# Optimization experiments

Measured on AMD Instinct MI355X. Metric: run time of the kernel, lower is better.

## Reference

```python
import jax, jax.numpy as jnp
import numpy as np

B, S, SE, D, H = 4, 1024, 256, 1536, 24
HD = D // H
EPS = 1e-5
STYLE_IDX = np.array([0, 0, 2, 2])  # expand_first: style stats of sample 0 -> {0,1}, sample 2 -> {2,3}


def adain(feat):
    # feat: [B,H,S,hd]; stats over seq dim (-2), unbiased var like torch
    m = feat.mean(axis=-2, keepdims=True)
    s = jnp.sqrt(feat.var(axis=-2, keepdims=True, ddof=1) + EPS)
    sm, ss = m[STYLE_IDX], s[STYLE_IDX]
    styled = (feat - m) / s * ss + sm
    # only batch indices 1 and 3 are restyled
    mask = jnp.array([0.0, 1.0, 0.0, 1.0], dtype=feat.dtype).reshape(B, 1, 1, 1)
    return feat * (1.0 - mask) + styled * mask


def heads(x):
    b, s, _ = x.shape
    return x.reshape(b, s, H, HD).transpose(0, 2, 1, 3)


def setup_inputs() -> dict:
    key = jax.random.key(0)
    ks = jax.random.split(key, 12)
    w = lambda k: jax.random.normal(k, (D, D), dtype=jnp.float32) * 0.02
    z = jnp.zeros((D,), dtype=jnp.float32)
    return {
        'hidden_states': jax.random.normal(ks[0], (B, S, D), dtype=jnp.float32),
        'encoder_hidden_states': jax.random.normal(ks[1], (B, SE, D), dtype=jnp.float32),
        'wq': w(ks[2]), 'bq': z, 'wk': w(ks[3]), 'bk': z, 'wv': w(ks[4]), 'bv': z,
        'awq': w(ks[5]), 'abq': z, 'awk': w(ks[6]), 'abk': z, 'awv': w(ks[7]), 'abv': z,
        'wo': w(ks[8]), 'bo': z, 'wao': w(ks[9]), 'bao': z,
    }


def reference(hidden_states, encoder_hidden_states, wq, bq, wk, bk, wv, bv,
              awq, abq, awk, abk, awv, abv, wo, bo, wao, bao):
    q = heads(hidden_states @ wq + bq)   # [B,H,S,hd]
    k = heads(hidden_states @ wk + bk)
    v = heads(hidden_states @ wv + bv)
    # adain_queries / adain_keys (adain_values=False)
    q = adain(q)
    k = adain(k)
    # share_attention: concat style K/V (scale=1.0 -> plain expand) along seq
    k = jnp.concatenate([k, k[STYLE_IDX]], axis=2)  # [B,H,2S,hd]
    v = jnp.concatenate([v, v[STYLE_IDX]], axis=2)
    # joint (text) streams
    eq = heads(encoder_hidden_states @ awq + abq)
    ek = heads(encoder_hidden_states @ awk + abk)
    ev = heads(encoder_hidden_states @ awv + abv)
    q = jnp.concatenate([q, eq], axis=2)   # [B,H,S+SE,hd]
    k = jnp.concatenate([k, ek], axis=2)   # [B,H,2S+SE,hd]
    v = jnp.concatenate([v, ev], axis=2)
    scale = 1.0 / np.sqrt(HD)
    logits = jnp.einsum('bhqd,bhkd->bhqk', q, k) * scale
    probs = jax.nn.softmax(logits, axis=-1)
    out = jnp.einsum('bhqk,bhkd->bhqd', probs, v)
    out = out.transpose(0, 2, 1, 3).reshape(B, -1, D)
    hid, enc = out[:, :S], out[:, S:]
    hid = hid @ wo + bo            # to_out[0] (to_out[1] is dropout/identity)
    enc = enc @ wao + bao          # to_add_out (context_pre_only=False)
    return hid, enc
```

## Files before the change

kernel.cpp:

```cpp
#include <hip/hip_runtime.h>
#include <hip/hip_bf16.h>


#define NB 4
#define NS 1024
#define NSE 256
#define ND 1536
#define NH 24
#define LK2 1280
#define SMAX 20.0f

typedef short bf16x8 __attribute__((ext_vector_type(8)));
typedef float f32x4 __attribute__((ext_vector_type(4)));

struct WPtrs { const float* w[8]; };
struct B6    { const float* p[6]; };

__device__ __forceinline__ unsigned short f2bf(float x) {
  union { float f; unsigned u; } a; a.f = x;
  unsigned r = a.u + 0x7fffu + ((a.u >> 16) & 1u);
  return (unsigned short)(r >> 16);
}
__device__ __forceinline__ void split2(float x, unsigned short& h, unsigned short& l) {
  union { float f; unsigned u; } a; a.f = x;
  h = (unsigned short)(a.u >> 16);
  union { float f; unsigned u; } b; b.u = a.u & 0xffff0000u;
  union { float f; unsigned u; } c; c.f = x - b.f;
  l = (unsigned short)(c.u >> 16);
}

__device__ __forceinline__ void gload_lds16(const unsigned short* g, unsigned short* l) {
  __builtin_amdgcn_global_load_lds(
      (const __attribute__((address_space(1))) void*)g,
      (__attribute__((address_space(3))) void*)l, 16, 0, 0);
}

__global__ __launch_bounds__(256) void conv_split_all(
    const float* __restrict__ hs, const float* __restrict__ ehs,
    unsigned short* __restrict__ HSh, unsigned short* __restrict__ HSl,
    unsigned short* __restrict__ EHh, unsigned short* __restrict__ EHl)
{
  int i = blockIdx.x * 256 + threadIdx.x;
  const float4* src; ushort4 *dh, *dl; int j;
  if (i < 1572864) { src = (const float4*)hs; j = i; dh = (ushort4*)HSh; dl = (ushort4*)HSl; }
  else { j = i - 1572864; src = (const float4*)ehs; dh = (ushort4*)EHh; dl = (ushort4*)EHl; }
  float4 v = src[j];
  ushort4 h, lo;
  split2(v.x, h.x, lo.x); split2(v.y, h.y, lo.y);
  split2(v.z, h.z, lo.z); split2(v.w, h.w, lo.w);
  dh[j] = h; dl[j] = lo;
}

__global__ __launch_bounds__(256) void conv_wt_all(WPtrs wp,
                                                   unsigned short* __restrict__ Wsp)
{
  __shared__ float tile[32][33];
  const int z = blockIdx.z;
  const float* W = wp.w[z];
  unsigned short* Th = Wsp + (long)(2 * z) * 2359296;
  unsigned short* Tl = Th + 2359296;
  const int k0 = blockIdx.x * 32, n0 = blockIdx.y * 32;
  const int r = threadIdx.x >> 5, c = threadIdx.x & 31;
#pragma unroll
  for (int i = 0; i < 4; ++i)
    tile[r + 8 * i][c] = W[(long)(k0 + r + 8 * i) * ND + n0 + c];
  __syncthreads();
#pragma unroll
  for (int i = 0; i < 4; ++i) {
    float v = tile[c][r + 8 * i];
    long o = (long)(n0 + r + 8 * i) * ND + k0 + c;
    unsigned short h, l;
    split2(v, h, l);
    Th[o] = h; Tl[o] = l;
  }
}

__device__ __forceinline__ void gemm_mfma_body(
    const unsigned short* __restrict__ Ah, const unsigned short* __restrict__ Al,
    const unsigned short* __restrict__ Bh, const unsigned short* __restrict__ Bl,
    const float* __restrict__ bias, float* __restrict__ C, int m0, int n0,
    bool third)
{
  __shared__ unsigned short sAh[128 * 32], sAl[128 * 32];
  __shared__ unsigned short sBh[128 * 32], sBl[128 * 32];

  const int t = threadIdx.x;
  const int w = t >> 6, l = t & 63;

  const int lr = l >> 2;
  const int lc = (l & 3) * 8;

  const unsigned short* pAh = Ah + (long)(m0 + 32 * w + lr) * ND + lc;
  const unsigned short* pAl = Al + (long)(m0 + 32 * w + lr) * ND + lc;
  const unsigned short* pBh = Bh + (long)(n0 + 32 * w + lr) * ND + lc;
  const unsigned short* pBl = Bl + (long)(n0 + 32 * w + lr) * ND + lc;

  unsigned short* qAh0 = &sAh[(32 * w) * 32];
  unsigned short* qAh1 = &sAh[(32 * w + 16) * 32];
  unsigned short* qAl0 = &sAl[(32 * w) * 32];
  unsigned short* qAl1 = &sAl[(32 * w + 16) * 32];
  unsigned short* qBh0 = &sBh[(32 * w) * 32];
  unsigned short* qBh1 = &sBh[(32 * w + 16) * 32];
  unsigned short* qBl0 = &sBl[(32 * w) * 32];
  unsigned short* qBl1 = &sBl[(32 * w + 16) * 32];

  const int rowA = (w >> 1) * 64 + (l & 15);
  const int rowB = (w & 1) * 64 + (l & 15);
  const int ko = (l >> 4) * 8;

  f32x4 acc[4][4] = {};

  for (int k0 = 0; k0 < ND; k0 += 32) {
    gload_lds16(pAh, qAh0);
    gload_lds16(pAh + 16 * ND, qAh1);
    if (third) {
      gload_lds16(pAl, qAl0);
      gload_lds16(pAl + 16 * ND, qAl1);
    }
    gload_lds16(pBh, qBh0);
    gload_lds16(pBh + 16 * ND, qBh1);
    gload_lds16(pBl, qBl0);
    gload_lds16(pBl + 16 * ND, qBl1);
    pAh += 32; pAl += 32; pBh += 32; pBl += 32;
    __syncthreads();

    bf16x8 fah[4], fal[4], fbh[4], fbl[4];
#pragma unroll
    for (int mt = 0; mt < 4; ++mt)
      fah[mt] = *(const bf16x8*)&sAh[(rowA + mt * 16) * 32 + ko];
    if (third) {
#pragma unroll
      for (int mt = 0; mt < 4; ++mt)
        fal[mt] = *(const bf16x8*)&sAl[(rowA + mt * 16) * 32 + ko];
    }
#pragma unroll
    for (int nt = 0; nt < 4; ++nt) {
      fbh[nt] = *(const bf16x8*)&sBh[(rowB + nt * 16) * 32 + ko];
      fbl[nt] = *(const bf16x8*)&sBl[(rowB + nt * 16) * 32 + ko];
    }
#pragma unroll
    for (int mt = 0; mt < 4; ++mt)
#pragma unroll
      for (int nt = 0; nt < 4; ++nt) {
        acc[mt][nt] = __builtin_amdgcn_mfma_f32_16x16x32_bf16(fah[mt], fbh[nt], acc[mt][nt], 0, 0, 0);
        acc[mt][nt] = __builtin_amdgcn_mfma_f32_16x16x32_bf16(fah[mt], fbl[nt], acc[mt][nt], 0, 0, 0);
      }
    if (third) {
#pragma unroll
      for (int mt = 0; mt < 4; ++mt)
#pragma unroll
        for (int nt = 0; nt < 4; ++nt)
          acc[mt][nt] = __builtin_amdgcn_mfma_f32_16x16x32_bf16(fal[mt], fbh[nt], acc[mt][nt], 0, 0, 0);
    }
    __syncthreads();
  }

  const int col0 = n0 + (w & 1) * 64 + (l & 15);
  const int row0 = m0 + (w >> 1) * 64 + (l >> 4) * 4;
#pragma unroll
  for (int nt = 0; nt < 4; ++nt) {
    float bv = bias[col0 + nt * 16];
#pragma unroll
    for (int mt = 0; mt < 4; ++mt)
#pragma unroll
      for (int r = 0; r < 4; ++r)
        C[(long)(row0 + mt * 16 + r) * ND + col0 + nt * 16] = acc[mt][nt][r] + bv;
  }
}

__global__ __launch_bounds__(256) void gemm3_all(
    const unsigned short* __restrict__ HSh, const unsigned short* __restrict__ HSl,
    const unsigned short* __restrict__ EHh, const unsigned short* __restrict__ EHl,
    const unsigned short* __restrict__ Wsp, B6 biases,
    float* __restrict__ Qb, float* __restrict__ EQb)
{
  const int z = blockIdx.z, y = blockIdx.y;
  const unsigned short *Ah, *Al;
  float* C;
  int m0, widx;
  if (y < 32) { Ah = HSh; Al = HSl; m0 = y * 128; widx = z;
                C = Qb + (long)z * 6291456; }
  else        { Ah = EHh; Al = EHl; m0 = (y - 32) * 128; widx = 3 + z;
                C = EQb + (long)z * 1572864; }
  const unsigned short* Bh = Wsp + (long)(2 * widx) * 2359296;
  const unsigned short* Bl = Bh + 2359296;
  gemm_mfma_body(Ah, Al, Bh, Bl, biases.p[widx], C, m0, blockIdx.x * 128,
                 z == 2);
}

__global__ __launch_bounds__(256) void gemm_out_all(
    const unsigned short* __restrict__ AOh,
    const unsigned short* __restrict__ Wsp,
    const float* __restrict__ bo, const float* __restrict__ bao,
    float* __restrict__ out)
{
  const int z = blockIdx.z, y = blockIdx.y;
  const unsigned short *Ah, *Bh, *Bl;
  const float* bias;
  float* C;
  int m0;
  if (y < 8) {
    Ah = AOh + (long)z * 1966080;
    m0 = y * 128;
    Bh = Wsp + (long)12 * 2359296; Bl = Bh + 2359296;
    bias = bo; C = out + (long)z * 1572864;
  } else {
    Ah = AOh + 1572864 + (long)z * 1966080;
    m0 = (y - 8) * 128;
    Bh = Wsp + (long)14 * 2359296; Bl = Bh + 2359296;
    bias = bao; C = out + 6291456 + (long)z * 393216;
  }
  gemm_mfma_body(Ah, Ah, Bh, Bl, bias, C, m0, blockIdx.x * 128, false);
}

__global__ __launch_bounds__(256) void adain_stats2(
    const float* __restrict__ Qb, const float* __restrict__ Kb,
    float* __restrict__ stm, float* __restrict__ sts,
    float* __restrict__ stm2, float* __restrict__ sts2)
{
  const float* X = blockIdx.z ? Kb : Qb;
  float* meanb = blockIdx.z ? stm2 : stm;
  float* sigb  = blockIdx.z ? sts2 : sts;
  const int b  = blockIdx.x;
  const int t  = threadIdx.x;
  const int dl = t & 63;
  const int sg = t >> 6;
  const int d  = blockIdx.y * 64 + dl;
  const float* xp = X + (long)b * NS * ND + d;
  float sum = 0.f, sq = 0.f;
  for (int s = sg; s < NS; s += 4) {
    float v = xp[(long)s * ND];
    sum += v; sq += v * v;
  }
  __shared__ float ss[4][64], s2[4][64];
  ss[sg][dl] = sum; s2[sg][dl] = sq;
  __syncthreads();
  if (t < 64) {
    float tot = ss[0][t] + ss[1][t] + ss[2][t] + ss[3][t];
    float tq  = s2[0][t] + s2[1][t] + s2[2][t] + s2[3][t];
    float mean = tot * (1.f / 1024.f);
    float var  = (tq - tot * mean) * (1.f / 1023.f);
    meanb[b * ND + blockIdx.y * 64 + t] = mean;
    sigb [b * ND + blockIdx.y * 64 + t] = sqrtf(var + 1e-5f);
  }
}

__global__ __launch_bounds__(256) void conv_KV(
    const float* __restrict__ Kf, const float* __restrict__ EKf,
    const float* __restrict__ Vf, const float* __restrict__ EVf,
    const float* __restrict__ stm2, const float* __restrict__ sts2,
    unsigned short* __restrict__ Kh, unsigned short* __restrict__ Kl,
    unsigned short* __restrict__ VT)
{
  __shared__ float tile[64][65];
  const int bh = blockIdx.y, b = bh / NH, h = bh - b * NH;
  if (blockIdx.x < 20) {
    const int key = blockIdx.x * 64 + (threadIdx.x >> 2);
    const int dc = (threadIdx.x & 3) * 16;
    const bool kad = ((b & 1) != 0) && (key < NS);
    const int srcb = b & 2;
    const float* src = (key < NS)
        ? Kf  + ((long)b * NS + key) * ND + h * 64 + dc
        : EKf + ((long)b * NSE + key - NS) * ND + h * 64 + dc;
    unsigned short* dh = Kh + ((long)bh * LK2 + key) * 64 + dc;
    unsigned short* dl = Kl + ((long)bh * LK2 + key) * 64 + dc;
    const long sb = (long)b * ND + h * 64 + dc;
    const long ss = (long)srcb * ND + h * 64 + dc;
#pragma unroll
    for (int i = 0; i < 4; ++i) {
      float4 v = *(const float4*)(src + 4 * i);
      if (kad) {
        float4 mb = *(const float4*)(stm2 + sb + 4 * i);
        float4 gb = *(const float4*)(sts2 + sb + 4 * i);
        float4 ms = *(const float4*)(stm2 + ss + 4 * i);
        float4 gs = *(const float4*)(sts2 + ss + 4 * i);
        v.x = (v.x - mb.x) * (gs.x / gb.x) + ms.x;
        v.y = (v.y - mb.y) * (gs.y / gb.y) + ms.y;
        v.z = (v.z - mb.z) * (gs.z / gb.z) + ms.z;
        v.w = (v.w - mb.w) * (gs.w / gb.w) + ms.w;
      }
      ushort4 hi, lo;
      split2(v.x, hi.x, lo.x); split2(v.y, hi.y, lo.y);
      split2(v.z, hi.z, lo.z); split2(v.w, hi.w, lo.w);
      *(ushort4*)(dh + 4 * i) = hi;
      *(ushort4*)(dl + 4 * i) = lo;
    }
  } else {
    const int k0 = (blockIdx.x - 20) * 64;
    {
      const int kl_ = threadIdx.x >> 2, dc = (threadIdx.x & 3) * 16;
      const int key = k0 + kl_;
      const float* src = (key < NS)
          ? Vf  + ((long)b * NS + key) * ND + h * 64 + dc
          : EVf + ((long)b * NSE + key - NS) * ND + h * 64 + dc;
#pragma unroll
      for (int i = 0; i < 4; ++i) {
        float4 v = *(const float4*)(src + 4 * i);
        tile[kl_][dc + 4 * i + 0] = v.x; tile[kl_][dc + 4 * i + 1] = v.y;
        tile[kl_][dc + 4 * i + 2] = v.z; tile[kl_][dc + 4 * i + 3] = v.w;
      }
    }
    __syncthreads();
    const int d = threadIdx.x >> 2, kc = (threadIdx.x & 3) * 16;
    unsigned short* dst = VT + ((long)bh * 64 + d) * LK2 + k0 + kc;
#pragma unroll
    for (int i = 0; i < 4; ++i) {
      ushort4 o4;
      o4.x = f2bf(tile[kc + 4 * i + 0][d]);
      o4.y = f2bf(tile[kc + 4 * i + 1][d]);
      o4.z = f2bf(tile[kc + 4 * i + 2][d]);
      o4.w = f2bf(tile[kc + 4 * i + 3][d]);
      *(ushort4*)(dst + 4 * i) = o4;
    }
  }
}

__global__ __launch_bounds__(256) void attn_mfma(
    const float* __restrict__ Q, const float* __restrict__ EQ,
    const unsigned short* __restrict__ Khg, const unsigned short* __restrict__ Klg,
    const unsigned short* __restrict__ VTg,
    const float* __restrict__ stm, const float* __restrict__ sts,
    unsigned short* __restrict__ AOh)
{
  __shared__ unsigned short sKh[2][64 * 64], sKl[2][64 * 64], sVT[2][64 * 64];
  __shared__ unsigned short sPh[64 * 72], sPl[64 * 72];

  const int t = threadIdx.x, w = t >> 6, l = t & 63;
  const int bh = blockIdx.y, b = bh / NH, h = bh - b * NH;
  const int bhs = (b & 2) * NH + h;
  const int q0 = blockIdx.x * 64;
  const int m = l & 15, g = l >> 4;
  const bool beven = (b & 1) == 0;
  const int nIter = beven ? 20 : 36;

  union FU { bf16x8 v; unsigned short u[8]; };
  FU qh[2], ql[2];
  {
    const bool qad = !beven && (q0 < NS);
    const int srcb = b & 2;
    const float* qrow = (q0 < NS)
        ? (Q  + ((long)b * NS + q0 + 16 * w + m) * ND + h * 64)
        : (EQ + ((long)b * NSE + (q0 - NS) + 16 * w + m) * ND + h * 64);
#pragma unroll
    for (int ks = 0; ks < 2; ++ks) {
      const int d0 = h * 64 + ks * 32 + g * 8;
      const float* p = qrow + ks * 32 + g * 8;
      float4 v0 = *(const float4*)p, v1 = *(const float4*)(p + 4);
      float vv[8] = {v0.x, v0.y, v0.z, v0.w, v1.x, v1.y, v1.z, v1.w};
      if (qad) {
        float4 mb0 = *(const float4*)(stm + (long)b * ND + d0);
        float4 mb1 = *(const float4*)(stm + (long)b * ND + d0 + 4);
        float4 gb0 = *(const float4*)(sts + (long)b * ND + d0);
        float4 gb1 = *(const float4*)(sts + (long)b * ND + d0 + 4);
        float4 ms0 = *(const float4*)(stm + (long)srcb * ND + d0);
        float4 ms1 = *(const float4*)(stm + (long)srcb * ND + d0 + 4);
        float4 gs0 = *(const float4*)(sts + (long)srcb * ND + d0);
        float4 gs1 = *(const float4*)(sts + (long)srcb * ND + d0 + 4);
        float mb[8] = {mb0.x, mb0.y, mb0.z, mb0.w, mb1.x, mb1.y, mb1.z, mb1.w};
        float gb[8] = {gb0.x, gb0.y, gb0.z, gb0.w, gb1.x, gb1.y, gb1.z, gb1.w};
        float ms[8] = {ms0.x, ms0.y, ms0.z, ms0.w, ms1.x, ms1.y, ms1.z, ms1.w};
        float gs[8] = {gs0.x, gs0.y, gs0.z, gs0.w, gs1.x, gs1.y, gs1.z, gs1.w};
#pragma unroll
        for (int j = 0; j < 8; ++j)
          vv[j] = (vv[j] - mb[j]) * (gs[j] / gb[j]) + ms[j];
      }
#pragma unroll
      for (int j = 0; j < 8; ++j)
        split2(vv[j] * 0.125f, qh[ks].u[j], ql[ks].u[j]);
    }
  }

  const int srow = l >> 3;
  const int sp = l & 7;
  const int osw = (sp - srow) & 7;
  const long ownK = (long)bh * LK2 * 64, styK = (long)bhs * LK2 * 64;
  const long ownV = (long)bh * 64 * LK2, styV = (long)bhs * 64 * LK2;
  const int offK = (16 * w + srow) * 64 + osw * 8;
  const int offV = (16 * w + srow) * LK2 + osw * 8;

  auto stage = [&](int kt, int bi) {
    int zone, j;
    if (beven) { zone = (kt < 16) ? 0 : 2; j = (kt < 16) ? kt : kt - 16; }
    else {
      zone = (kt < 16) ? 0 : ((kt < 32) ? 1 : 2);
      j = (kt < 16) ? kt : ((kt < 32) ? kt - 16 : kt - 32);
    }
    const long keyBase = ((zone == 2) ? 1024 : 0) + (long)j * 64;
    const unsigned short* kb = Khg + ((zone == 1) ? styK : ownK) + keyBase * 64;
    const unsigned short* lb = Klg + ((zone == 1) ? styK : ownK) + keyBase * 64;
    const unsigned short* vb = VTg + ((zone == 1) ? styV : ownV) + keyBase;
    gload_lds16(kb + offK, &sKh[bi][(16 * w) * 64]);
    gload_lds16(kb + 8 * 64 + offK, &sKh[bi][(16 * w + 8) * 64]);
    gload_lds16(lb + offK, &sKl[bi][(16 * w) * 64]);
    gload_lds16(lb + 8 * 64 + offK, &sKl[bi][(16 * w + 8) * 64]);
    gload_lds16(vb + offV, &sVT[bi][(16 * w) * 64]);
    gload_lds16(vb + 8 * LK2 + offV, &sVT[bi][(16 * w + 8) * 64]);
  };

  const int p0 = (g + m) & 7;
  const int p1 = (4 + g + m) & 7;

  f32x4 oacc[4] = {};
  float l_part[4] = {0.f, 0.f, 0.f, 0.f};

  stage(0, 0);

  for (int kt = 0; kt < nIter; ++kt) {
    const int cur = kt & 1;
    __syncthreads();
    if (kt + 1 < nIter) stage(kt + 1, cur ^ 1);

    const float ebias = (beven && kt < 16) ? (0.69314718f - SMAX) : (-SMAX);

    f32x4 sacc[4] = {};
#pragma unroll
    for (int ks = 0; ks < 2; ++ks) {
      const int pp = ks ? p1 : p0;
#pragma unroll
      for (int nt = 0; nt < 4; ++nt) {
        const int ak = (nt * 16 + m) * 64 + pp * 8;
        bf16x8 fkh = *(const bf16x8*)&sKh[cur][ak];
        bf16x8 fkl = *(const bf16x8*)&sKl[cur][ak];
        sacc[nt] = __builtin_amdgcn_mfma_f32_16x16x32_bf16(qh[ks].v, fkh, sacc[nt], 0, 0, 0);
        sacc[nt] = __builtin_amdgcn_mfma_f32_16x16x32_bf16(qh[ks].v, fkl, sacc[nt], 0, 0, 0);
        sacc[nt] = __builtin_amdgcn_mfma_f32_16x16x32_bf16(ql[ks].v, fkh, sacc[nt], 0, 0, 0);
      }
    }

#pragma unroll
    for (int nt = 0; nt < 4; ++nt)
#pragma unroll
      for (int r = 0; r < 4; ++r)
        sacc[nt][r] = __expf(sacc[nt][r] + ebias);
#pragma unroll
    for (int r = 0; r < 4; ++r)
      l_part[r] += (sacc[0][r] + sacc[1][r]) + (sacc[2][r] + sacc[3][r]);
#pragma unroll
    for (int nt = 0; nt < 4; ++nt)
#pragma unroll
      for (int r = 0; r < 4; ++r) {
        unsigned short ph, pl;
        split2(sacc[nt][r], ph, pl);
        const int ad = (16 * w + 4 * g + r) * 72 + nt * 16 + m;
        sPh[ad] = ph; sPl[ad] = pl;
      }

#pragma unroll
    for (int ks = 0; ks < 2; ++ks) {
      const int pp = ks ? p1 : p0;
      const int ap = (16 * w + m) * 72 + ks * 32 + g * 8;
      bf16x8 fph = *(const bf16x8*)&sPh[ap];
      bf16x8 fpl = *(const bf16x8*)&sPl[ap];
#pragma unroll
      for (int nt2 = 0; nt2 < 4; ++nt2) {
        const int av = (nt2 * 16 + m) * 64 + pp * 8;
        bf16x8 fv = *(const bf16x8*)&sVT[cur][av];
        oacc[nt2] = __builtin_amdgcn_mfma_f32_16x16x32_bf16(fph, fv, oacc[nt2], 0, 0, 0);
        oacc[nt2] = __builtin_amdgcn_mfma_f32_16x16x32_bf16(fpl, fv, oacc[nt2], 0, 0, 0);
      }
    }
  }

#pragma unroll
  for (int r = 0; r < 4; ++r) {
#pragma unroll
    for (int off = 1; off < 16; off <<= 1)
      l_part[r] += __shfl_xor(l_part[r], off, 16);
  }
#pragma unroll
  for (int r = 0; r < 4; ++r) {
    float inv = 1.f / l_part[r];
    const long row = (long)b * 1280 + q0 + 16 * w + 4 * g + r;
    const long base = row * ND + h * 64;
#pragma unroll
    for (int nt2 = 0; nt2 < 4; ++nt2)
      AOh[base + nt2 * 16 + m] = f2bf(oacc[nt2][r] * inv);
  }
}

extern "C" void kernel_launch(void* const* d_in, const int* in_sizes, int n_in,
                              void* d_out, int out_size, void* d_ws, size_t ws_size,
                              hipStream_t stream) {
  const float* hs  = (const float*)d_in[0];
  const float* ehs = (const float*)d_in[1];
  WPtrs wp;
  wp.w[0] = (const float*)d_in[2];  wp.w[1] = (const float*)d_in[4];
  wp.w[2] = (const float*)d_in[6];  wp.w[3] = (const float*)d_in[8];
  wp.w[4] = (const float*)d_in[10]; wp.w[5] = (const float*)d_in[12];
  wp.w[6] = (const float*)d_in[14]; wp.w[7] = (const float*)d_in[16];
  B6 biases;
  biases.p[0] = (const float*)d_in[3];
  biases.p[1] = (const float*)d_in[5];
  biases.p[2] = (const float*)d_in[7];
  biases.p[3] = (const float*)d_in[9];
  biases.p[4] = (const float*)d_in[11];
  biases.p[5] = (const float*)d_in[13];
  const float* bo  = (const float*)d_in[15];
  const float* bao = (const float*)d_in[17];
  float* out = (float*)d_out;

  float* Qb  = (float*)d_ws;
  float* Kb  = Qb  + 6291456;
  float* Vb  = Kb  + 6291456;
  float* EQb = Vb  + 6291456;
  float* EKb = EQb + 1572864;
  float* EVb = EKb + 1572864;
  float* stm  = EVb + 1572864;
  float* sts  = stm + 6144;
  float* stm2 = sts + 6144;
  float* sts2 = stm2 + 6144;
  unsigned short* U0  = (unsigned short*)(sts2 + 6144);
  unsigned short* HSh = U0;
  unsigned short* HSl = U0 + 6291456;
  unsigned short* EHh = U0 + 12582912;
  unsigned short* EHl = U0 + 14155776;
  unsigned short* AOh = U0;
  unsigned short* Wsp = U0 + 15728640;
  unsigned short* Khg = Wsp;
  unsigned short* Klg = Wsp + 7864320;
  unsigned short* VTg = Wsp + 15728640;

  dim3 blk(256);

  conv_split_all<<<7680, blk, 0, stream>>>(hs, ehs, HSh, HSl, EHh, EHl);
  conv_wt_all<<<dim3(48, 48, 8), blk, 0, stream>>>(wp, Wsp);

  gemm3_all<<<dim3(12, 40, 3), blk, 0, stream>>>(
      HSh, HSl, EHh, EHl, Wsp, biases, Qb, EQb);

  adain_stats2<<<dim3(4, 24, 2), blk, 0, stream>>>(Qb, Kb, stm, sts, stm2, sts2);

  conv_KV<<<dim3(40, 96), blk, 0, stream>>>(Kb, EKb, Vb, EVb, stm2, sts2,
                                            Khg, Klg, VTg);

  attn_mfma<<<dim3(20, 96), blk, 0, stream>>>(Qb, EQb, Khg, Klg, VTg,
                                              stm, sts, AOh);

  gemm_out_all<<<dim3(12, 10, 4), blk, 0, stream>>>(AOh, Wsp, bo, bao, out);
}
```

Baseline: 740.3 us.

## Remap attention grid for XCD load balance, use exp2 and MFMA priority hints

The attention launch becomes a 1D grid of 1920 blocks. Each block index is decoded so that consecutive groups of 8 blocks, which likely land on different XCDs, interleave light (even-batch, 20 tiles) and heavy (odd-batch, 36 tiles) work. This is meant to balance load across chiplets and keep related heads together for L2 reuse. The softmax now folds log2(e) into the Q scale and bias and calls the hardware exp2 directly, and s_setprio brackets raise wave priority around the MFMA sections. These add index arithmetic and depend on how the hardware dispatches blocks to XCDs.

```diff
diff --git a/kernel.cpp b/kernel.cpp
--- a/kernel.cpp
+++ b/kernel.cpp
@@ -9,6 +9,7 @@
 #define NH 24
 #define LK2 1280
 #define SMAX 20.0f
+#define LOG2E 1.44269504f
 
 typedef short bf16x8 __attribute__((ext_vector_type(8)));
 typedef float f32x4 __attribute__((ext_vector_type(4)));
@@ -326,9 +327,17 @@
   __shared__ unsigned short sPh[64 * 72], sPl[64 * 72];
 
   const int t = threadIdx.x, w = t >> 6, l = t & 63;
-  const int bh = blockIdx.y, b = bh / NH, h = bh - b * NH;
+  const int lin = blockIdx.x;
+  const int x = lin & 7;
+  const int j = lin >> 3;
+  const int parity = j & 1;
+  const int u = j >> 1;
+  const int i6 = 6 * x + u / 20;
+  const int q0 = (u % 20) * 64;
+  const int bh = parity ? (i6 < 24 ? i6 + 24 : i6 + 48)
+                        : (i6 < 24 ? i6      : i6 + 24);
+  const int b = bh / NH, h = bh - b * NH;
   const int bhs = (b & 2) * NH + h;
-  const int q0 = blockIdx.x * 64;
   const int m = l & 15, g = l >> 4;
   const bool beven = (b & 1) == 0;
   const int nIter = beven ? 20 : 36;
@@ -361,12 +370,12 @@
         float ms[8] = {ms0.x, ms0.y, ms0.z, ms0.w, ms1.x, ms1.y, ms1.z, ms1.w};
         float gs[8] = {gs0.x, gs0.y, gs0.z, gs0.w, gs1.x, gs1.y, gs1.z, gs1.w};
 #pragma unroll
-        for (int j = 0; j < 8; ++j)
-          vv[j] = (vv[j] - mb[j]) * (gs[j] / gb[j]) + ms[j];
-      }
-#pragma unroll
-      for (int j = 0; j < 8; ++j)
-        split2(vv[j] * 0.125f, qh[ks].u[j], ql[ks].u[j]);
+        for (int j2 = 0; j2 < 8; ++j2)
+          vv[j2] = (vv[j2] - mb[j2]) * (gs[j2] / gb[j2]) + ms[j2];
+      }
+#pragma unroll
+      for (int j2 = 0; j2 < 8; ++j2)
+        split2(vv[j2] * (0.125f * LOG2E), qh[ks].u[j2], ql[ks].u[j2]);
     }
   }
 
@@ -379,13 +388,13 @@
   const int offV = (16 * w + srow) * LK2 + osw * 8;
 
   auto stage = [&](int kt, int bi) {
-    int zone, j;
-    if (beven) { zone = (kt < 16) ? 0 : 2; j = (kt < 16) ? kt : kt - 16; }
+    int zone, jz;
+    if (beven) { zone = (kt < 16) ? 0 : 2; jz = (kt < 16) ? kt : kt - 16; }
     else {
       zone = (kt < 16) ? 0 : ((kt < 32) ? 1 : 2);
-      j = (kt < 16) ? kt : ((kt < 32) ? kt - 16 : kt - 32);
-    }
-    const long keyBase = ((zone == 2) ? 1024 : 0) + (long)j * 64;
+      jz = (kt < 16) ? kt : ((kt < 32) ? kt - 16 : kt - 32);
+    }
+    const long keyBase = ((zone == 2) ? 1024 : 0) + (long)jz * 64;
     const unsigned short* kb = Khg + ((zone == 1) ? styK : ownK) + keyBase * 64;
     const unsigned short* lb = Klg + ((zone == 1) ? styK : ownK) + keyBase * 64;
     const unsigned short* vb = VTg + ((zone == 1) ? styV : ownV) + keyBase;
@@ -410,9 +419,11 @@
     __syncthreads();
     if (kt + 1 < nIter) stage(kt + 1, cur ^ 1);
 
-    const float ebias = (beven && kt < 16) ? (0.69314718f - SMAX) : (-SMAX);
+    const float ebias = (beven && kt < 16) ? (1.0f - SMAX * LOG2E)
+                                           : (-SMAX * LOG2E);
 
     f32x4 sacc[4] = {};
+    __builtin_amdgcn_s_setprio(1);
 #pragma unroll
     for (int ks = 0; ks < 2; ++ks) {
       const int pp = ks ? p1 : p0;
@@ -426,12 +437,13 @@
         sacc[nt] = __builtin_amdgcn_mfma_f32_16x16x32_bf16(ql[ks].v, fkh, sacc[nt], 0, 0, 0);
       }
     }
+    __builtin_amdgcn_s_setprio(0);
 
 #pragma unroll
     for (int nt = 0; nt < 4; ++nt)
 #pragma unroll
       for (int r = 0; r < 4; ++r)
-        sacc[nt][r] = __expf(sacc[nt][r] + ebias);
+        sacc[nt][r] = __builtin_amdgcn_exp2f(sacc[nt][r] + ebias);
 #pragma unroll
     for (int r = 0; r < 4; ++r)
       l_part[r] += (sacc[0][r] + sacc[1][r]) + (sacc[2][r] + sacc[3][r]);
@@ -445,6 +457,7 @@
         sPh[ad] = ph; sPl[ad] = pl;
       }
 
+    __builtin_amdgcn_s_setprio(1);
 #pragma unroll
     for (int ks = 0; ks < 2; ++ks) {
       const int pp = ks ? p1 : p0;
@@ -459,6 +472,7 @@
         oacc[nt2] = __builtin_amdgcn_mfma_f32_16x16x32_bf16(fpl, fv, oacc[nt2], 0, 0, 0);
       }
     }
+    __builtin_amdgcn_s_setprio(0);
   }
 
 #pragma unroll
@@ -533,8 +547,8 @@
   conv_KV<<<dim3(40, 96), blk, 0, stream>>>(Kb, EKb, Vb, EVb, stm2, sts2,
                                             Khg, Klg, VTg);
 
-  attn_mfma<<<dim3(20, 96), blk, 0, stream>>>(Qb, EQb, Khg, Klg, VTg,
-                                              stm, sts, AOh);
+  attn_mfma<<<dim3(1920), blk, 0, stream>>>(Qb, EQb, Khg, Klg, VTg,
+                                            stm, sts, AOh);
 
   gemm_out_all<<<dim3(12, 10, 4), blk, 0, stream>>>(AOh, Wsp, bo, bao, out);
 }
```

Result: slower. 759.9 us (+2.7%).
